# Performance work log

Hardware: AMD Instinct MI355X
Metric: run time of the kernel (lower is better)

Reference implementation:

```python
import jax, jax.numpy as jnp
import numpy as np

N_SRC = 100000
N_DST = 20000
N_EDGES = 640000
D_IN = 128
D_OUT = 128


def setup_inputs() -> dict:
    key = jax.random.key(0)
    ks = jax.random.split(key, 6)
    feat_src = jax.random.normal(ks[0], (N_SRC, D_IN), dtype=jnp.float32)
    feat_dst = jax.random.normal(ks[1], (N_DST, D_IN), dtype=jnp.float32)
    src_idx = jax.random.randint(ks[2], (N_EDGES,), 0, N_SRC, dtype=jnp.int64 if jax.config.jax_enable_x64 else jnp.int32)
    dst_idx = jax.random.randint(ks[3], (N_EDGES,), 0, N_DST, dtype=jnp.int64 if jax.config.jax_enable_x64 else jnp.int32)
    # xavier-uniform-ish init scale for [out, in] Linear weights
    lim = float(np.sqrt(6.0 / (D_IN + D_OUT)))
    W_self = jax.random.uniform(ks[4], (D_OUT, D_IN), jnp.float32, -lim, lim)
    W_neigh = jax.random.uniform(ks[5], (D_OUT, D_IN), jnp.float32, -lim, lim)
    b_self = jnp.zeros((D_OUT,), jnp.float32)
    b_neigh = jnp.zeros((D_OUT,), jnp.float32)
    return {
        "feat_src": feat_src, "feat_dst": feat_dst,
        "src_idx": src_idx, "dst_idx": dst_idx,
        "W_self": W_self, "b_self": b_self,
        "W_neigh": W_neigh, "b_neigh": b_neigh,
    }


def reference(feat_src, feat_dst, src_idx, dst_idx, W_self, b_self, W_neigh, b_neigh):
    n_dst = feat_dst.shape[0]
    # message passing: copy_src + mean reduce over incoming edges per dst node
    msgs = feat_src[src_idx]                                   # [E, D_in]
    summed = jax.ops.segment_sum(msgs, dst_idx, num_segments=n_dst)  # [N_dst, D_in]
    deg = jax.ops.segment_sum(jnp.ones((src_idx.shape[0],), feat_src.dtype),
                              dst_idx, num_segments=n_dst)     # [N_dst]
    h_neigh = summed / jnp.maximum(deg, 1.0)[:, None]          # mean (0 for isolated)
    # rst = fc_self(h_self) + fc_neigh(h_neigh); no activation
    rst = (feat_dst @ W_self.T + b_self) + (h_neigh @ W_neigh.T + b_neigh)
    return rst
```

## Files before the change

### kernel.cpp

```cpp
#include <hip/hip_runtime.h>

#define D 128
#define NDST 20000
#define NB 256
#define CAP 96

typedef __attribute__((ext_vector_type(8))) short short8;
typedef __attribute__((ext_vector_type(4))) float f32x4;
typedef __attribute__((ext_vector_type(2))) float f32x2;

__device__ __forceinline__ unsigned f2bf(float f) {
  unsigned x = __float_as_uint(f);
  return (x + 0x7FFFu + ((x >> 16) & 1u)) >> 16;
}
__device__ __forceinline__ unsigned pack2(float a, float b) {
  return f2bf(a) | (f2bf(b) << 16);
}
__device__ __forceinline__ unsigned pack_fp8x4(float a, float b, float c, float d) {
  int v = 0;
  v = __builtin_amdgcn_cvt_pk_fp8_f32(a, b, v, false);
  v = __builtin_amdgcn_cvt_pk_fp8_f32(c, d, v, true);
  return (unsigned)v;
}

__global__ __launch_bounds__(512) void p1(
    const int* __restrict__ dst_idx,
    const float* __restrict__ feat_src,
    unsigned char* __restrict__ blockHist8,
    unsigned short* __restrict__ rank16,
    unsigned char* __restrict__ fsrc8,
    const float* __restrict__ W_self, const float* __restrict__ W_neigh,
    unsigned short* __restrict__ Wcat,
    int n_src, int n_edges, int EPB, int NCB)
{
  const int tid = threadIdx.x;
  const int bid = blockIdx.x;

  if (bid < NB) {
    __shared__ unsigned int hist[NDST / 4];
    for (int i = tid; i < NDST / 16; i += 512)
      reinterpret_cast<uint4*>(hist)[i] = make_uint4(0u, 0u, 0u, 0u);
    __syncthreads();
    const int e0 = bid * EPB;
    const int e1 = min(e0 + EPB, n_edges);
    for (int e = e0 + tid; e < e1; e += 512) {
      int d = dst_idx[e];
      int sh = (d & 3) << 3;
      unsigned old = atomicAdd(&hist[d >> 2], 1u << sh);
      rank16[e] = (unsigned short)((old >> sh) & 0xFFu);
    }
    __syncthreads();
    uint4* rowp = reinterpret_cast<uint4*>(blockHist8 + (size_t)bid * NDST);
    const uint4* h4 = reinterpret_cast<const uint4*>(hist);
    for (int i = tid; i < NDST / 16; i += 512) rowp[i] = h4[i];
  } else if (bid < NB + 8) {
    int u = (bid - NB) * 512 + tid;
    int l = u * 8;
    int n = l >> 8;
    int k0 = l & 255;
    const float* src = (k0 < D) ? (W_self + n * D + k0)
                                : (W_neigh + n * D + (k0 - D));
    const float4* p = reinterpret_cast<const float4*>(src);
    float4 a = p[0], b = p[1];
    uint4 o;
    o.x = pack2(a.x, a.y); o.y = pack2(a.z, a.w);
    o.z = pack2(b.x, b.y); o.w = pack2(b.z, b.w);
    *reinterpret_cast<uint4*>(Wcat + (size_t)n * 256 + k0) = o;
  } else {
    const long long NCONV = (long long)n_src * 16;
    const long long NU = NCONV + 16;
    const long long stride = (long long)NCB * 512;
    long long u = (long long)(bid - NB - 8) * 512 + tid;
    for (; u < NU; u += stride) {
      if (u < NCONV) {
        long long e = u * 8;
        const float4* p = reinterpret_cast<const float4*>(feat_src + e);
        float4 a = p[0], b = p[1];
        uint2 o;
        o.x = pack_fp8x4(a.x, a.y, a.z, a.w);
        o.y = pack_fp8x4(b.x, b.y, b.z, b.w);
        *reinterpret_cast<uint2*>(fsrc8 + e) = o;
      } else {
        *reinterpret_cast<uint2*>(fsrc8 + (size_t)n_src * D + (u - NCONV) * 8) =
            make_uint2(0u, 0u);
      }
    }
  }
}

__global__ __launch_bounds__(256) void pB(
    unsigned char* __restrict__ blockHist8,
    int* __restrict__ degi,
    int n_dst)
{
  int d = blockIdx.x * 256 + threadIdx.x;
  if (d >= n_dst) return;
  unsigned char* col = blockHist8 + d;
  unsigned run = 0;
  #pragma unroll 8
  for (int b = 0; b < NB; ++b) {
    unsigned h = col[(size_t)b * NDST];
    col[(size_t)b * NDST] = (unsigned char)run;
    run += h;
  }
  degi[d] = (int)run;
}

__global__ __launch_bounds__(256) void p3(
    const int* __restrict__ src_idx,
    const int* __restrict__ dst_idx,
    const unsigned short* __restrict__ rank16,
    const unsigned char* __restrict__ blockBase8,
    int* __restrict__ bucket,
    int n_edges, int EPB)
{
  int e0 = (blockIdx.x * 256 + threadIdx.x) * 4;
  if (e0 >= n_edges) return;
  if (e0 + 4 <= n_edges) {
    int4 s4 = *reinterpret_cast<const int4*>(src_idx + e0);
    int4 d4 = *reinterpret_cast<const int4*>(dst_idx + e0);
    ushort4 r4 = *reinterpret_cast<const ushort4*>(rank16 + e0);
    int ds[4] = {d4.x, d4.y, d4.z, d4.w};
    int ss[4] = {s4.x, s4.y, s4.z, s4.w};
    unsigned rr[4] = {r4.x, r4.y, r4.z, r4.w};
    #pragma unroll
    for (int j = 0; j < 4; ++j) {
      int hb = (e0 + j) / EPB;
      unsigned slot = (unsigned)blockBase8[(size_t)hb * NDST + ds[j]] + rr[j];
      if (slot < CAP) bucket[(size_t)ds[j] * CAP + slot] = ss[j];
    }
  } else {
    for (int e = e0; e < n_edges; ++e) {
      int d = dst_idx[e];
      int hb = e / EPB;
      unsigned slot = (unsigned)blockBase8[(size_t)hb * NDST + d] + rank16[e];
      if (slot < CAP) bucket[(size_t)d * CAP + slot] = src_idx[e];
    }
  }
}

__global__ __launch_bounds__(512) void fused_tail(
    const unsigned char* __restrict__ fsrc8,
    const int* __restrict__ degi,
    const int* __restrict__ bucket,
    const float* __restrict__ feat_dst,
    const unsigned short* __restrict__ Wcat,
    const float* __restrict__ b_self,
    const float* __restrict__ b_neigh,
    float* __restrict__ out,
    int n_src, int n_dst)
{
  __shared__ unsigned short Af[32][136];
  __shared__ unsigned short Ah[32][136];
  __shared__ unsigned short Bs[128][136];

  const int tid  = threadIdx.x;
  const int w    = tid >> 6;
  const int lane = tid & 63;
  const int row0 = blockIdx.x * 32;

  {
    int r = tid >> 4;
    int q = tid & 15;
    int gr = row0 + r;
    uint4 o = make_uint4(0u, 0u, 0u, 0u);
    if (gr < n_dst) {
      const float4* p = reinterpret_cast<const float4*>(
          feat_dst + (size_t)gr * D + q * 8);
      float4 a = p[0], b = p[1];
      o.x = pack2(a.x, a.y); o.y = pack2(a.z, a.w);
      o.z = pack2(b.x, b.y); o.w = pack2(b.z, b.w);
    }
    *reinterpret_cast<uint4*>(&Af[r][q * 8]) = o;
  }

  {
    const int g = lane >> 4;
    const int c = lane & 15;
    const uint2* fs2 = reinterpret_cast<const uint2*>(fsrc8);

    for (int it = 0; it < 4; ++it) {
      int row = w * 4 + it;
      int gr = row0 + row;
      if (gr >= n_dst) {
        if (lane < 16)
          *reinterpret_cast<uint4*>(&Ah[row][c * 8]) = make_uint4(0u,0u,0u,0u);
        continue;
      }
      const int total = degi[gr];
      const int use = min(total, CAP);
      const int* brow = bucket + (size_t)gr * CAP;

      float acc[8];
      #pragma unroll
      for (int j = 0; j < 8; ++j) acc[j] = 0.f;

      for (int i = g; i < use; i += 16) {
        int s0 = brow[i];
        int s1 = (i + 4  < use) ? brow[i + 4]  : n_src;
        int s2 = (i + 8  < use) ? brow[i + 8]  : n_src;
        int s3 = (i + 12 < use) ? brow[i + 12] : n_src;
        uint2 v0 = fs2[(size_t)s0 * 16 + c];
        uint2 v1 = fs2[(size_t)s1 * 16 + c];
        uint2 v2 = fs2[(size_t)s2 * 16 + c];
        uint2 v3 = fs2[(size_t)s3 * 16 + c];
        #pragma unroll
        for (int k = 0; k < 4; ++k) {
          unsigned wx = (k == 0) ? v0.x : (k == 1) ? v1.x : (k == 2) ? v2.x : v3.x;
          unsigned wy = (k == 0) ? v0.y : (k == 1) ? v1.y : (k == 2) ? v2.y : v3.y;
          f32x2 a0 = __builtin_amdgcn_cvt_pk_f32_fp8(wx, false);
          f32x2 a1 = __builtin_amdgcn_cvt_pk_f32_fp8(wx, true);
          f32x2 a2 = __builtin_amdgcn_cvt_pk_f32_fp8(wy, false);
          f32x2 a3 = __builtin_amdgcn_cvt_pk_f32_fp8(wy, true);
          acc[0] += a0.x; acc[1] += a0.y; acc[2] += a1.x; acc[3] += a1.y;
          acc[4] += a2.x; acc[5] += a2.y; acc[6] += a3.x; acc[7] += a3.y;
        }
      }

      #pragma unroll
      for (int j = 0; j < 8; ++j) {
        acc[j] += __shfl_xor(acc[j], 16);
        acc[j] += __shfl_xor(acc[j], 32);
      }

      if (lane < 16) {
        float inv = 1.0f / fmaxf((float)total, 1.0f);
        uint4 o;
        o.x = pack2(acc[0] * inv, acc[1] * inv);
        o.y = pack2(acc[2] * inv, acc[3] * inv);
        o.z = pack2(acc[4] * inv, acc[5] * inv);
        o.w = pack2(acc[6] * inv, acc[7] * inv);
        *reinterpret_cast<uint4*>(&Ah[row][c * 8]) = o;
      }
    }
  }

  const int m  = w & 1;
  const int n0 = (w >> 1) * 2;
  const int ar = m * 16 + (lane & 15);
  const int kb = (lane >> 4) * 8;

  f32x4 acc2[2];
  acc2[0] = (f32x4){0.f, 0.f, 0.f, 0.f};
  acc2[1] = (f32x4){0.f, 0.f, 0.f, 0.f};

  #pragma unroll
  for (int kc = 0; kc < 2; ++kc) {
    __syncthreads();
    {
      int n = tid >> 2;
      int q = tid & 3;
      const uint4* p = reinterpret_cast<const uint4*>(
          Wcat + (size_t)n * 256 + kc * 128 + q * 32);
      uint4 v0 = p[0], v1 = p[1], v2 = p[2], v3 = p[3];
      *reinterpret_cast<uint4*>(&Bs[n][q * 32 + 0])  = v0;
      *reinterpret_cast<uint4*>(&Bs[n][q * 32 + 8])  = v1;
      *reinterpret_cast<uint4*>(&Bs[n][q * 32 + 16]) = v2;
      *reinterpret_cast<uint4*>(&Bs[n][q * 32 + 24]) = v3;
    }
    __syncthreads();

    const unsigned short (*Asrc)[136] = (kc == 0) ? Af : Ah;
    #pragma unroll
    for (int kh = 0; kh < 4; ++kh) {
      short8 a = *reinterpret_cast<const short8*>(&Asrc[ar][kh * 32 + kb]);
      #pragma unroll
      for (int t2 = 0; t2 < 2; ++t2) {
        short8 b = *reinterpret_cast<const short8*>(
            &Bs[(n0 + t2) * 16 + (lane & 15)][kh * 32 + kb]);
        acc2[t2] = __builtin_amdgcn_mfma_f32_16x16x32_bf16(a, b, acc2[t2], 0, 0, 0);
      }
    }
  }

  const int r0 = row0 + m * 16 + (lane >> 4) * 4;
  #pragma unroll
  for (int t2 = 0; t2 < 2; ++t2) {
    int col = (n0 + t2) * 16 + (lane & 15);
    float bv = b_self[col] + b_neigh[col];
    #pragma unroll
    for (int r = 0; r < 4; ++r) {
      int gr = r0 + r;
      if (gr < n_dst) out[(size_t)gr * D + col] = acc2[t2][r] + bv;
    }
  }
}

extern "C" void kernel_launch(void* const* d_in, const int* in_sizes, int n_in,
                              void* d_out, int out_size, void* d_ws, size_t ws_size,
                              hipStream_t stream) {
  const float* feat_src = (const float*)d_in[0];
  const float* feat_dst = (const float*)d_in[1];
  const int*   src_idx  = (const int*)d_in[2];
  const int*   dst_idx  = (const int*)d_in[3];
  const float* W_self   = (const float*)d_in[4];
  const float* b_self   = (const float*)d_in[5];
  const float* W_neigh  = (const float*)d_in[6];
  const float* b_neigh  = (const float*)d_in[7];
  float* out = (float*)d_out;

  const int n_src   = in_sizes[0] / D;
  const int n_dst   = in_sizes[1] / D;
  const int n_edges = in_sizes[2];

  unsigned char* fsrc8 = (unsigned char*)d_ws;
  unsigned short* Wcat = (unsigned short*)(fsrc8 + (size_t)(n_src + 1) * D);
  int* degi   = (int*)(Wcat + 128 * 256);
  int* bucket = degi + NDST;
  unsigned short* rank16 = (unsigned short*)(bucket + (size_t)NDST * CAP);
  unsigned char* blockHist8 = (unsigned char*)(rank16 + n_edges);

  const int EPB = (n_edges + NB - 1) / NB;
  const int NCB = 256;

  p1<<<NB + 8 + NCB, 512, 0, stream>>>(
      dst_idx, feat_src, blockHist8, rank16, fsrc8, W_self, W_neigh, Wcat,
      n_src, n_edges, EPB, NCB);

  pB<<<(n_dst + 255) / 256, 256, 0, stream>>>(blockHist8, degi, n_dst);

  p3<<<(n_edges / 4 + 255) / 256, 256, 0, stream>>>(
      src_idx, dst_idx, rank16, blockHist8, bucket, n_edges, EPB);

  fused_tail<<<(n_dst + 31) / 32, 512, 0, stream>>>(
      fsrc8, degi, bucket, feat_dst, Wcat, b_self, b_neigh, out,
      n_src, n_dst);
}
```

Baseline: 67.95 us.

## Move self-projection GEMM into first kernel and shrink histogram block count

The feat_dst @ W_self GEMM and bias add move into extra blocks of the first kernel, so they overlap with the histogram and fp8 conversion work. The tail then only computes the neighbor GEMM and adds it into out. The Wcat pre-pack is removed: each GEMM block converts W_self or W_neigh to bf16 itself. The histogram block count drops from 256 to 64, which shortens the column scan in pB. The costs are an extra read-modify-write of out, redundant per-block weight conversion, and a 43.5KB static LDS allocation that every k1 block carries, which may reduce occupancy for the conversion blocks.

```diff
diff --git a/kernel.cpp b/kernel.cpp
--- a/kernel.cpp
+++ b/kernel.cpp
@@ -2,7 +2,7 @@
 
 #define D 128
 #define NDST 20000
-#define NB 256
+#define NHB 64
 #define CAP 96
 
 typedef __attribute__((ext_vector_type(8))) short short8;
@@ -23,21 +23,25 @@
   return (unsigned)v;
 }
 
-__global__ __launch_bounds__(512) void p1(
+__global__ __launch_bounds__(512) void k1(
     const int* __restrict__ dst_idx,
     const float* __restrict__ feat_src,
+    const float* __restrict__ feat_dst,
+    const float* __restrict__ W_self,
+    const float* __restrict__ b_self,
+    const float* __restrict__ b_neigh,
     unsigned char* __restrict__ blockHist8,
     unsigned short* __restrict__ rank16,
     unsigned char* __restrict__ fsrc8,
-    const float* __restrict__ W_self, const float* __restrict__ W_neigh,
-    unsigned short* __restrict__ Wcat,
-    int n_src, int n_edges, int EPB, int NCB)
+    float* __restrict__ out,
+    int n_src, int n_dst, int n_edges, int EPB, int NCB)
 {
+  __shared__ __align__(16) unsigned char ldsb[43520];
   const int tid = threadIdx.x;
   const int bid = blockIdx.x;
 
-  if (bid < NB) {
-    __shared__ unsigned int hist[NDST / 4];
+  if (bid < NHB) {
+    unsigned int* hist = reinterpret_cast<unsigned int*>(ldsb);
     for (int i = tid; i < NDST / 16; i += 512)
       reinterpret_cast<uint4*>(hist)[i] = make_uint4(0u, 0u, 0u, 0u);
     __syncthreads();
@@ -53,24 +57,11 @@
     uint4* rowp = reinterpret_cast<uint4*>(blockHist8 + (size_t)bid * NDST);
     const uint4* h4 = reinterpret_cast<const uint4*>(hist);
     for (int i = tid; i < NDST / 16; i += 512) rowp[i] = h4[i];
-  } else if (bid < NB + 8) {
-    int u = (bid - NB) * 512 + tid;
-    int l = u * 8;
-    int n = l >> 8;
-    int k0 = l & 255;
-    const float* src = (k0 < D) ? (W_self + n * D + k0)
-                                : (W_neigh + n * D + (k0 - D));
-    const float4* p = reinterpret_cast<const float4*>(src);
-    float4 a = p[0], b = p[1];
-    uint4 o;
-    o.x = pack2(a.x, a.y); o.y = pack2(a.z, a.w);
-    o.z = pack2(b.x, b.y); o.w = pack2(b.z, b.w);
-    *reinterpret_cast<uint4*>(Wcat + (size_t)n * 256 + k0) = o;
-  } else {
+  } else if (bid < NHB + NCB) {
     const long long NCONV = (long long)n_src * 16;
     const long long NU = NCONV + 16;
     const long long stride = (long long)NCB * 512;
-    long long u = (long long)(bid - NB - 8) * 512 + tid;
+    long long u = (long long)(bid - NHB) * 512 + tid;
     for (; u < NU; u += stride) {
       if (u < NCONV) {
         long long e = u * 8;
@@ -85,6 +76,72 @@
             make_uint2(0u, 0u);
       }
     }
+  } else {
+    unsigned short (*As)[136] = reinterpret_cast<unsigned short (*)[136]>(ldsb);
+    unsigned short (*Bs)[136] =
+        reinterpret_cast<unsigned short (*)[136]>(ldsb + 32 * 136 * 2);
+    const int w = tid >> 6;
+    const int lane = tid & 63;
+    const int row0 = (bid - NHB - NCB) * 32;
+
+    {
+      int r = tid >> 4;
+      int q = tid & 15;
+      int gr = row0 + r;
+      uint4 o = make_uint4(0u, 0u, 0u, 0u);
+      if (gr < n_dst) {
+        const float4* p = reinterpret_cast<const float4*>(
+            feat_dst + (size_t)gr * D + q * 8);
+        float4 a = p[0], b = p[1];
+        o.x = pack2(a.x, a.y); o.y = pack2(a.z, a.w);
+        o.z = pack2(b.x, b.y); o.w = pack2(b.z, b.w);
+      }
+      *reinterpret_cast<uint4*>(&As[r][q * 8]) = o;
+    }
+    {
+      int n = tid >> 2;
+      int q = tid & 3;
+      const float4* p = reinterpret_cast<const float4*>(
+          W_self + (size_t)n * D + q * 32);
+      #pragma unroll
+      for (int h = 0; h < 4; ++h) {
+        float4 a = p[2 * h], b = p[2 * h + 1];
+        uint4 o;
+        o.x = pack2(a.x, a.y); o.y = pack2(a.z, a.w);
+        o.z = pack2(b.x, b.y); o.w = pack2(b.z, b.w);
+        *reinterpret_cast<uint4*>(&Bs[n][q * 32 + h * 8]) = o;
+      }
+    }
+    __syncthreads();
+
+    const int m  = w & 1;
+    const int n0 = (w >> 1) * 2;
+    const int ar = m * 16 + (lane & 15);
+    const int kb = (lane >> 4) * 8;
+    f32x4 acc2[2];
+    acc2[0] = (f32x4){0.f, 0.f, 0.f, 0.f};
+    acc2[1] = (f32x4){0.f, 0.f, 0.f, 0.f};
+    #pragma unroll
+    for (int kh = 0; kh < 4; ++kh) {
+      short8 a = *reinterpret_cast<const short8*>(&As[ar][kh * 32 + kb]);
+      #pragma unroll
+      for (int t2 = 0; t2 < 2; ++t2) {
+        short8 b = *reinterpret_cast<const short8*>(
+            &Bs[(n0 + t2) * 16 + (lane & 15)][kh * 32 + kb]);
+        acc2[t2] = __builtin_amdgcn_mfma_f32_16x16x32_bf16(a, b, acc2[t2], 0, 0, 0);
+      }
+    }
+    const int r0 = row0 + m * 16 + (lane >> 4) * 4;
+    #pragma unroll
+    for (int t2 = 0; t2 < 2; ++t2) {
+      int col = (n0 + t2) * 16 + (lane & 15);
+      float bv = b_self[col] + b_neigh[col];
+      #pragma unroll
+      for (int r = 0; r < 4; ++r) {
+        int gr = r0 + r;
+        if (gr < n_dst) out[(size_t)gr * D + col] = acc2[t2][r] + bv;
+      }
+    }
   }
 }
 
@@ -98,7 +155,7 @@
   unsigned char* col = blockHist8 + d;
   unsigned run = 0;
   #pragma unroll 8
-  for (int b = 0; b < NB; ++b) {
+  for (int b = 0; b < NHB; ++b) {
     unsigned h = col[(size_t)b * NDST];
     col[(size_t)b * NDST] = (unsigned char)run;
     run += h;
@@ -139,18 +196,14 @@
   }
 }
 
-__global__ __launch_bounds__(512) void fused_tail(
+__global__ __launch_bounds__(512) void tail(
     const unsigned char* __restrict__ fsrc8,
     const int* __restrict__ degi,
     const int* __restrict__ bucket,
-    const float* __restrict__ feat_dst,
-    const unsigned short* __restrict__ Wcat,
-    const float* __restrict__ b_self,
-    const float* __restrict__ b_neigh,
+    const float* __restrict__ W_neigh,
     float* __restrict__ out,
     int n_src, int n_dst)
 {
-  __shared__ unsigned short Af[32][136];
   __shared__ unsigned short Ah[32][136];
   __shared__ unsigned short Bs[128][136];
 
@@ -158,21 +211,6 @@
   const int w    = tid >> 6;
   const int lane = tid & 63;
   const int row0 = blockIdx.x * 32;
-
-  {
-    int r = tid >> 4;
-    int q = tid & 15;
-    int gr = row0 + r;
-    uint4 o = make_uint4(0u, 0u, 0u, 0u);
-    if (gr < n_dst) {
-      const float4* p = reinterpret_cast<const float4*>(
-          feat_dst + (size_t)gr * D + q * 8);
-      float4 a = p[0], b = p[1];
-      o.x = pack2(a.x, a.y); o.y = pack2(a.z, a.w);
-      o.z = pack2(b.x, b.y); o.w = pack2(b.z, b.w);
-    }
-    *reinterpret_cast<uint4*>(&Af[r][q * 8]) = o;
-  }
 
   {
     const int g = lane >> 4;
@@ -234,6 +272,23 @@
       }
     }
   }
+  __syncthreads();
+
+  {
+    int n = tid >> 2;
+    int q = tid & 3;
+    const float4* p = reinterpret_cast<const float4*>(
+        W_neigh + (size_t)n * D + q * 32);
+    #pragma unroll
+    for (int h = 0; h < 4; ++h) {
+      float4 a = p[2 * h], b = p[2 * h + 1];
+      uint4 o;
+      o.x = pack2(a.x, a.y); o.y = pack2(a.z, a.w);
+      o.z = pack2(b.x, b.y); o.w = pack2(b.z, b.w);
+      *reinterpret_cast<uint4*>(&Bs[n][q * 32 + h * 8]) = o;
+    }
+  }
+  __syncthreads();
 
   const int m  = w & 1;
   const int n0 = (w >> 1) * 2;
@@ -245,31 +300,13 @@
   acc2[1] = (f32x4){0.f, 0.f, 0.f, 0.f};
 
   #pragma unroll
-  for (int kc = 0; kc < 2; ++kc) {
-    __syncthreads();
-    {
-      int n = tid >> 2;
-      int q = tid & 3;
-      const uint4* p = reinterpret_cast<const uint4*>(
-          Wcat + (size_t)n * 256 + kc * 128 + q * 32);
-      uint4 v0 = p[0], v1 = p[1], v2 = p[2], v3 = p[3];
-      *reinterpret_cast<uint4*>(&Bs[n][q * 32 + 0])  = v0;
-      *reinterpret_cast<uint4*>(&Bs[n][q * 32 + 8])  = v1;
-      *reinterpret_cast<uint4*>(&Bs[n][q * 32 + 16]) = v2;
-      *reinterpret_cast<uint4*>(&Bs[n][q * 32 + 24]) = v3;
-    }
-    __syncthreads();
-
-    const unsigned short (*Asrc)[136] = (kc == 0) ? Af : Ah;
-    #pragma unroll
-    for (int kh = 0; kh < 4; ++kh) {
-      short8 a = *reinterpret_cast<const short8*>(&Asrc[ar][kh * 32 + kb]);
-      #pragma unroll
-      for (int t2 = 0; t2 < 2; ++t2) {
-        short8 b = *reinterpret_cast<const short8*>(
-            &Bs[(n0 + t2) * 16 + (lane & 15)][kh * 32 + kb]);
-        acc2[t2] = __builtin_amdgcn_mfma_f32_16x16x32_bf16(a, b, acc2[t2], 0, 0, 0);
-      }
+  for (int kh = 0; kh < 4; ++kh) {
+    short8 a = *reinterpret_cast<const short8*>(&Ah[ar][kh * 32 + kb]);
+    #pragma unroll
+    for (int t2 = 0; t2 < 2; ++t2) {
+      short8 b = *reinterpret_cast<const short8*>(
+          &Bs[(n0 + t2) * 16 + (lane & 15)][kh * 32 + kb]);
+      acc2[t2] = __builtin_amdgcn_mfma_f32_16x16x32_bf16(a, b, acc2[t2], 0, 0, 0);
     }
   }
 
@@ -277,11 +314,13 @@
   #pragma unroll
   for (int t2 = 0; t2 < 2; ++t2) {
     int col = (n0 + t2) * 16 + (lane & 15);
-    float bv = b_self[col] + b_neigh[col];
     #pragma unroll
     for (int r = 0; r < 4; ++r) {
       int gr = r0 + r;
-      if (gr < n_dst) out[(size_t)gr * D + col] = acc2[t2][r] + bv;
+      if (gr < n_dst) {
+        size_t idx = (size_t)gr * D + col;
+        out[idx] = out[idx] + acc2[t2][r];
+      }
     }
   }
 }
@@ -304,25 +343,24 @@
   const int n_edges = in_sizes[2];
 
   unsigned char* fsrc8 = (unsigned char*)d_ws;
-  unsigned short* Wcat = (unsigned short*)(fsrc8 + (size_t)(n_src + 1) * D);
-  int* degi   = (int*)(Wcat + 128 * 256);
+  int* degi   = (int*)(fsrc8 + (size_t)(n_src + 1) * D);
   int* bucket = degi + NDST;
   unsigned short* rank16 = (unsigned short*)(bucket + (size_t)NDST * CAP);
   unsigned char* blockHist8 = (unsigned char*)(rank16 + n_edges);
 
-  const int EPB = (n_edges + NB - 1) / NB;
+  const int EPB = (n_edges + NHB - 1) / NHB;
   const int NCB = 256;
-
-  p1<<<NB + 8 + NCB, 512, 0, stream>>>(
-      dst_idx, feat_src, blockHist8, rank16, fsrc8, W_self, W_neigh, Wcat,
-      n_src, n_edges, EPB, NCB);
+  const int NG  = (n_dst + 31) / 32;
+
+  k1<<<NHB + NCB + NG, 512, 0, stream>>>(
+      dst_idx, feat_src, feat_dst, W_self, b_self, b_neigh,
+      blockHist8, rank16, fsrc8, out, n_src, n_dst, n_edges, EPB, NCB);
 
   pB<<<(n_dst + 255) / 256, 256, 0, stream>>>(blockHist8, degi, n_dst);
 
   p3<<<(n_edges / 4 + 255) / 256, 256, 0, stream>>>(
       src_idx, dst_idx, rank16, blockHist8, bucket, n_edges, EPB);
 
-  fused_tail<<<(n_dst + 31) / 32, 512, 0, stream>>>(
-      fsrc8, degi, bucket, feat_dst, Wcat, b_self, b_neigh, out,
-      n_src, n_dst);
-}
+  tail<<<NG, 512, 0, stream>>>(
+      fsrc8, degi, bucket, W_neigh, out, n_src, n_dst);
+}
```

Result: faster. 66.17 us (-2.6%).

## Merge histogram, scan and bucket scatter into one cooperative kernel

Applied to the files above, without the earlier changes.

Replaces three separate preprocessing launches (histogram/convert, column prefix scan, bucket scatter) with one cooperative kernel that separates the phases with grid-wide syncs. The number of histogram blocks drops from 256 to 64, so the per-destination prefix scan walks fewer rows. Weight bf16 conversion now happens inside the tail kernel from fp32 weights, removing the Wcat staging buffer. The aim is to cut launch gaps and scan traffic. In exchange it pays grid-sync latency, heavier per-block atomic histogramming, and redundant weight conversion in every tail block.

```diff
diff --git a/kernel.cpp b/kernel.cpp
--- a/kernel.cpp
+++ b/kernel.cpp
@@ -1,8 +1,12 @@
 #include <hip/hip_runtime.h>
+#include <hip/hip_cooperative_groups.h>
+
+namespace cg = cooperative_groups;
 
 #define D 128
 #define NDST 20000
-#define NB 256
+#define NHB 64
+#define NBLK 512
 #define CAP 96
 
 typedef __attribute__((ext_vector_type(8))) short short8;
@@ -23,21 +27,23 @@
   return (unsigned)v;
 }
 
-__global__ __launch_bounds__(512) void p1(
+__global__ __launch_bounds__(512, 4) void mega(
+    const int* __restrict__ src_idx,
     const int* __restrict__ dst_idx,
     const float* __restrict__ feat_src,
     unsigned char* __restrict__ blockHist8,
     unsigned short* __restrict__ rank16,
     unsigned char* __restrict__ fsrc8,
-    const float* __restrict__ W_self, const float* __restrict__ W_neigh,
-    unsigned short* __restrict__ Wcat,
-    int n_src, int n_edges, int EPB, int NCB)
+    int* __restrict__ bucket,
+    int* __restrict__ degi,
+    int n_src, int n_dst, int n_edges, int EPB)
 {
+  cg::grid_group grid = cg::this_grid();
+  __shared__ unsigned int hist[NDST / 4];
   const int tid = threadIdx.x;
   const int bid = blockIdx.x;
 
-  if (bid < NB) {
-    __shared__ unsigned int hist[NDST / 4];
+  if (bid < NHB) {
     for (int i = tid; i < NDST / 16; i += 512)
       reinterpret_cast<uint4*>(hist)[i] = make_uint4(0u, 0u, 0u, 0u);
     __syncthreads();
@@ -53,24 +59,11 @@
     uint4* rowp = reinterpret_cast<uint4*>(blockHist8 + (size_t)bid * NDST);
     const uint4* h4 = reinterpret_cast<const uint4*>(hist);
     for (int i = tid; i < NDST / 16; i += 512) rowp[i] = h4[i];
-  } else if (bid < NB + 8) {
-    int u = (bid - NB) * 512 + tid;
-    int l = u * 8;
-    int n = l >> 8;
-    int k0 = l & 255;
-    const float* src = (k0 < D) ? (W_self + n * D + k0)
-                                : (W_neigh + n * D + (k0 - D));
-    const float4* p = reinterpret_cast<const float4*>(src);
-    float4 a = p[0], b = p[1];
-    uint4 o;
-    o.x = pack2(a.x, a.y); o.y = pack2(a.z, a.w);
-    o.z = pack2(b.x, b.y); o.w = pack2(b.z, b.w);
-    *reinterpret_cast<uint4*>(Wcat + (size_t)n * 256 + k0) = o;
   } else {
     const long long NCONV = (long long)n_src * 16;
     const long long NU = NCONV + 16;
-    const long long stride = (long long)NCB * 512;
-    long long u = (long long)(bid - NB - 8) * 512 + tid;
+    const long long stride = (long long)(NBLK - NHB) * 512;
+    long long u = (long long)(bid - NHB) * 512 + tid;
     for (; u < NU; u += stride) {
       if (u < NCONV) {
         long long e = u * 8;
@@ -86,65 +79,60 @@
       }
     }
   }
-}
-
-__global__ __launch_bounds__(256) void pB(
-    unsigned char* __restrict__ blockHist8,
-    int* __restrict__ degi,
-    int n_dst)
-{
-  int d = blockIdx.x * 256 + threadIdx.x;
-  if (d >= n_dst) return;
-  unsigned char* col = blockHist8 + d;
-  unsigned run = 0;
-  #pragma unroll 8
-  for (int b = 0; b < NB; ++b) {
-    unsigned h = col[(size_t)b * NDST];
-    col[(size_t)b * NDST] = (unsigned char)run;
-    run += h;
-  }
-  degi[d] = (int)run;
-}
-
-__global__ __launch_bounds__(256) void p3(
-    const int* __restrict__ src_idx,
-    const int* __restrict__ dst_idx,
-    const unsigned short* __restrict__ rank16,
-    const unsigned char* __restrict__ blockBase8,
-    int* __restrict__ bucket,
-    int n_edges, int EPB)
-{
-  int e0 = (blockIdx.x * 256 + threadIdx.x) * 4;
-  if (e0 >= n_edges) return;
-  if (e0 + 4 <= n_edges) {
-    int4 s4 = *reinterpret_cast<const int4*>(src_idx + e0);
-    int4 d4 = *reinterpret_cast<const int4*>(dst_idx + e0);
-    ushort4 r4 = *reinterpret_cast<const ushort4*>(rank16 + e0);
-    int ds[4] = {d4.x, d4.y, d4.z, d4.w};
-    int ss[4] = {s4.x, s4.y, s4.z, s4.w};
-    unsigned rr[4] = {r4.x, r4.y, r4.z, r4.w};
-    #pragma unroll
-    for (int j = 0; j < 4; ++j) {
-      int hb = (e0 + j) / EPB;
-      unsigned slot = (unsigned)blockBase8[(size_t)hb * NDST + ds[j]] + rr[j];
-      if (slot < CAP) bucket[(size_t)ds[j] * CAP + slot] = ss[j];
-    }
-  } else {
-    for (int e = e0; e < n_edges; ++e) {
-      int d = dst_idx[e];
-      int hb = e / EPB;
-      unsigned slot = (unsigned)blockBase8[(size_t)hb * NDST + d] + rank16[e];
-      if (slot < CAP) bucket[(size_t)d * CAP + slot] = src_idx[e];
-    }
-  }
-}
-
-__global__ __launch_bounds__(512) void fused_tail(
+  grid.sync();
+
+  {
+    int d = bid * 512 + tid;
+    if (d < n_dst) {
+      unsigned char* col = blockHist8 + d;
+      unsigned run = 0;
+      #pragma unroll 8
+      for (int b = 0; b < NHB; ++b) {
+        unsigned h = col[(size_t)b * NDST];
+        col[(size_t)b * NDST] = (unsigned char)run;
+        run += h;
+      }
+      degi[d] = (int)run;
+    }
+  }
+  grid.sync();
+
+  {
+    const int nq = (n_edges + 3) / 4;
+    for (int q = bid * 512 + tid; q < nq; q += NBLK * 512) {
+      int e0 = q * 4;
+      if (e0 + 4 <= n_edges) {
+        int4 s4 = *reinterpret_cast<const int4*>(src_idx + e0);
+        int4 d4 = *reinterpret_cast<const int4*>(dst_idx + e0);
+        ushort4 r4 = *reinterpret_cast<const ushort4*>(rank16 + e0);
+        int ds[4] = {d4.x, d4.y, d4.z, d4.w};
+        int ss[4] = {s4.x, s4.y, s4.z, s4.w};
+        unsigned rr[4] = {r4.x, r4.y, r4.z, r4.w};
+        #pragma unroll
+        for (int j = 0; j < 4; ++j) {
+          int hb = (e0 + j) / EPB;
+          unsigned slot = (unsigned)blockHist8[(size_t)hb * NDST + ds[j]] + rr[j];
+          if (slot < CAP) bucket[(size_t)ds[j] * CAP + slot] = ss[j];
+        }
+      } else {
+        for (int e = e0; e < n_edges; ++e) {
+          int d = dst_idx[e];
+          int hb = e / EPB;
+          unsigned slot = (unsigned)blockHist8[(size_t)hb * NDST + d] + rank16[e];
+          if (slot < CAP) bucket[(size_t)d * CAP + slot] = src_idx[e];
+        }
+      }
+    }
+  }
+}
+
+__global__ __launch_bounds__(512) void tail(
     const unsigned char* __restrict__ fsrc8,
     const int* __restrict__ degi,
     const int* __restrict__ bucket,
     const float* __restrict__ feat_dst,
-    const unsigned short* __restrict__ Wcat,
+    const float* __restrict__ W_self,
+    const float* __restrict__ W_neigh,
     const float* __restrict__ b_self,
     const float* __restrict__ b_neigh,
     float* __restrict__ out,
@@ -248,15 +236,19 @@
   for (int kc = 0; kc < 2; ++kc) {
     __syncthreads();
     {
+      const float* W = (kc == 0) ? W_self : W_neigh;
       int n = tid >> 2;
       int q = tid & 3;
-      const uint4* p = reinterpret_cast<const uint4*>(
-          Wcat + (size_t)n * 256 + kc * 128 + q * 32);
-      uint4 v0 = p[0], v1 = p[1], v2 = p[2], v3 = p[3];
-      *reinterpret_cast<uint4*>(&Bs[n][q * 32 + 0])  = v0;
-      *reinterpret_cast<uint4*>(&Bs[n][q * 32 + 8])  = v1;
-      *reinterpret_cast<uint4*>(&Bs[n][q * 32 + 16]) = v2;
-      *reinterpret_cast<uint4*>(&Bs[n][q * 32 + 24]) = v3;
+      const float4* p = reinterpret_cast<const float4*>(
+          W + (size_t)n * D + q * 32);
+      #pragma unroll
+      for (int h = 0; h < 4; ++h) {
+        float4 a = p[2 * h], b = p[2 * h + 1];
+        uint4 o;
+        o.x = pack2(a.x, a.y); o.y = pack2(a.z, a.w);
+        o.z = pack2(b.x, b.y); o.w = pack2(b.z, b.w);
+        *reinterpret_cast<uint4*>(&Bs[n][q * 32 + h * 8]) = o;
+      }
     }
     __syncthreads();
 
@@ -299,30 +291,27 @@
   const float* b_neigh  = (const float*)d_in[7];
   float* out = (float*)d_out;
 
-  const int n_src   = in_sizes[0] / D;
-  const int n_dst   = in_sizes[1] / D;
-  const int n_edges = in_sizes[2];
+  int n_src   = in_sizes[0] / D;
+  int n_dst   = in_sizes[1] / D;
+  int n_edges = in_sizes[2];
 
   unsigned char* fsrc8 = (unsigned char*)d_ws;
-  unsigned short* Wcat = (unsigned short*)(fsrc8 + (size_t)(n_src + 1) * D);
-  int* degi   = (int*)(Wcat + 128 * 256);
+  int* degi   = (int*)(fsrc8 + (size_t)(n_src + 1) * D);
   int* bucket = degi + NDST;
   unsigned short* rank16 = (unsigned short*)(bucket + (size_t)NDST * CAP);
   unsigned char* blockHist8 = (unsigned char*)(rank16 + n_edges);
 
-  const int EPB = (n_edges + NB - 1) / NB;
-  const int NCB = 256;
-
-  p1<<<NB + 8 + NCB, 512, 0, stream>>>(
-      dst_idx, feat_src, blockHist8, rank16, fsrc8, W_self, W_neigh, Wcat,
-      n_src, n_edges, EPB, NCB);
-
-  pB<<<(n_dst + 255) / 256, 256, 0, stream>>>(blockHist8, degi, n_dst);
-
-  p3<<<(n_edges / 4 + 255) / 256, 256, 0, stream>>>(
-      src_idx, dst_idx, rank16, blockHist8, bucket, n_edges, EPB);
-
-  fused_tail<<<(n_dst + 31) / 32, 512, 0, stream>>>(
-      fsrc8, degi, bucket, feat_dst, Wcat, b_self, b_neigh, out,
+  int EPB = (n_edges + NHB - 1) / NHB;
+
+  void* args[] = {
+    (void*)&src_idx, (void*)&dst_idx, (void*)&feat_src,
+    (void*)&blockHist8, (void*)&rank16, (void*)&fsrc8,
+    (void*)&bucket, (void*)&degi,
+    (void*)&n_src, (void*)&n_dst, (void*)&n_edges, (void*)&EPB
+  };
+  hipLaunchCooperativeKernel((void*)mega, dim3(NBLK), dim3(512), args, 0, stream);
+
+  tail<<<(n_dst + 31) / 32, 512, 0, stream>>>(
+      fsrc8, degi, bucket, feat_dst, W_self, W_neigh, b_self, b_neigh, out,
       n_src, n_dst);
 }
```

New measurement: 207.4 us. +205.2%, slower.
